# Performance work log

Measured on AMD Instinct MI355X. Metric: run time of the kernel, lower is better.

## Reference

```python
import jax, jax.numpy as jnp
import numpy as np

K = 4  # number of neighbors, per kNN-VC convention

def setup_inputs() -> dict:
    key = jax.random.key(0)
    k1, k2 = jax.random.split(key)
    source_feats = jax.random.normal(k1, (2048, 1024), dtype=jnp.float32)
    target_feats = jax.random.normal(k2, (50000, 1024), dtype=jnp.float32)
    return {"source_feats": source_feats, "target_feats": target_feats}

def reference(source_feats, target_feats):
    # cosine kNN matching: for each source frame, find K nearest target frames
    # under cosine distance (= highest cosine similarity), then average them.
    eps = jnp.asarray(1e-8, source_feats.dtype)
    src_n = source_feats / jnp.maximum(jnp.linalg.norm(source_feats, axis=-1, keepdims=True), eps)
    tgt_n = target_feats / jnp.maximum(jnp.linalg.norm(target_feats, axis=-1, keepdims=True), eps)
    # [T_src, T_tgt] cosine similarity
    sims = jnp.einsum('sd,td->st', src_n, tgt_n)
    _, idx = jax.lax.top_k(sims, K)          # [T_src, K]
    neighbors = target_feats[idx]             # [T_src, K, D]
    out = jnp.mean(neighbors, axis=1)         # [T_src, D]
    return out
```

## Files before the change

kernel.cpp:

```cpp
#include <hip/hip_runtime.h>
#include <math.h>

#define S_ROWS 2048
#define T_ROWS 50000
#define DIM    1024
#define KNN    4

#define BM 128
#define BN 128
#define KBB 128
#define TILES_PER_CHUNK 4
#define CHUNK_COLS (BN * TILES_PER_CHUNK)
#define NUM_CHUNKS ((T_ROWS + CHUNK_COLS - 1) / CHUNK_COLS)
#define T_PAD (NUM_CHUNKS * CHUNK_COLS)
#define NCAND (NUM_CHUNKS * KNN)
#define REFINE 16
#define SP 67
#define QSCALE 500.0f

typedef unsigned int uint;
typedef unsigned long long u64;
typedef signed char i8;
typedef __attribute__((ext_vector_type(4))) int i32x4;

__device__ __forceinline__ u64 packI(int v, int idx) {
  return ((u64)((uint)v ^ 0x80000000u) << 32) | (uint)(~idx);
}

template <int N>
__device__ __forceinline__ void insU(u64 p, u64 (&tv)[N]) {
  if (p <= tv[N - 1]) return;
  tv[N - 1] = p;
#pragma unroll
  for (int j = N - 1; j > 0; --j) {
    if (tv[j] > tv[j - 1]) { u64 t = tv[j]; tv[j] = tv[j - 1]; tv[j - 1] = t; }
  }
}

__device__ __forceinline__ void llds16(const void* g, void* l) {
  __builtin_amdgcn_global_load_lds(
      reinterpret_cast<__attribute__((address_space(1))) void*>(
          reinterpret_cast<uintptr_t>(g)),
      reinterpret_cast<__attribute__((address_space(3))) void*>(
          (unsigned)reinterpret_cast<uintptr_t>(l)),
      16, 0, 0);
}

__device__ __forceinline__ int imax2(int a, int b) { return a > b ? a : b; }

__global__ __launch_bounds__(256) void quant_kernel(const float* __restrict__ in,
                                                    i8* __restrict__ outq, int nvalid) {
  const int row = blockIdx.x;
  const int tid = threadIdx.x;
  if (row >= nvalid) {
    ((uint*)(outq + ((size_t)row << 10)))[tid] = 0u;
    return;
  }
  __shared__ float red[4];
  float4 v = ((const float4*)(in + ((size_t)row << 10)))[tid];
  float s = v.x * v.x + v.y * v.y + v.z * v.z + v.w * v.w;
#pragma unroll
  for (int off = 32; off; off >>= 1) s += __shfl_down(s, off, 64);
  if ((tid & 63) == 0) red[tid >> 6] = s;
  __syncthreads();
  float tot = red[0] + red[1] + red[2] + red[3];
  float r = QSCALE / fmaxf(sqrtf(tot), 1e-8f);
  int q0 = __float2int_rn(v.x * r), q1 = __float2int_rn(v.y * r);
  int q2 = __float2int_rn(v.z * r), q3 = __float2int_rn(v.w * r);
  q0 = imax2(-127, (q0 < 127 ? q0 : 127));
  q1 = imax2(-127, (q1 < 127 ? q1 : 127));
  q2 = imax2(-127, (q2 < 127 ? q2 : 127));
  q3 = imax2(-127, (q3 < 127 ? q3 : 127));
  uint packed = ((uint)q0 & 255u) | (((uint)q1 & 255u) << 8) |
                (((uint)q2 & 255u) << 16) | (((uint)q3 & 255u) << 24);
  ((uint*)(outq + ((size_t)row << 10)))[tid] = packed;
}

union __align__(16) SimSmem {
  i8 ab[2][BM * KBB];
  int sims[BM * SP];
  u64 mb[256 * KNN];
};

__global__ __launch_bounds__(256) void sim_i8_kernel(const i8* __restrict__ srcq,
                                                     const i8* __restrict__ tgtq,
                                                     u64* __restrict__ partials) {
  __shared__ SimSmem sm;
  i8* sA = sm.ab[0];
  i8* sB = sm.ab[1];

  const int tid = threadIdx.x;
  const int lane = tid & 63;
  const int wave = tid >> 6;
  const int qr = (wave >> 1) * 64;
  const int qch = wave & 1;
  const int m = lane & 15;
  const int quad = lane >> 4;
  const int r0 = blockIdx.x * BM;
  const int chunk = blockIdx.y;

  const int srow8 = lane >> 3;
  const int scb = (lane & 7) ^ srow8;
  const i8* aBase = srcq + (((size_t)(r0 + wave * 32 + srow8)) << 10) + scb * 16;
  i8* aL = sA + wave * 4096;
  i8* bL = sB + wave * 4096;

  const int axor = m & 7;
  const int aoff = (qr + m) * KBB;
  const int boff = (qch * 64 + m) * KBB;

  u64 topp[KNN] = {0, 0, 0, 0};
  int thrI = (int)0x80000000;

  for (int tile = 0; tile < TILES_PER_CHUNK; ++tile) {
    const int c0 = chunk * CHUNK_COLS + tile * BN;
    const i8* bBase = tgtq + (((size_t)(c0 + wave * 32 + srow8)) << 10) + scb * 16;

    i32x4 acc[4][4];
#pragma unroll
    for (int i = 0; i < 4; ++i)
#pragma unroll
      for (int j = 0; j < 4; ++j) acc[i][j] = (i32x4){0, 0, 0, 0};

    for (int kb = 0; kb < DIM; kb += KBB) {
#pragma unroll
      for (int d = 0; d < 4; ++d) {
        llds16(aBase + kb + d * 8192, aL + d * 1024);
        llds16(bBase + kb + d * 8192, bL + d * 1024);
      }
      __syncthreads();
#pragma unroll
      for (int s = 0; s < 2; ++s) {
        const int bpos = ((s * 4 + quad) ^ axor) * 16;
        i32x4 af[4], bf[4];
#pragma unroll
        for (int i = 0; i < 4; ++i)
          af[i] = *(const i32x4*)(sA + aoff + i * (16 * KBB) + bpos);
#pragma unroll
        for (int j = 0; j < 4; ++j)
          bf[j] = *(const i32x4*)(sB + boff + j * (16 * KBB) + bpos);
#pragma unroll
        for (int i = 0; i < 4; ++i)
#pragma unroll
          for (int j = 0; j < 4; ++j)
            acc[i][j] = __builtin_amdgcn_mfma_i32_16x16x64_i8(af[i], bf[j], acc[i][j], 0, 0, 0);
      }
      __syncthreads();
    }

#pragma unroll
    for (int ph = 0; ph < 2; ++ph) {
      if (qch == ph) {
#pragma unroll
        for (int i = 0; i < 4; ++i)
#pragma unroll
          for (int j = 0; j < 4; ++j)
#pragma unroll
            for (int reg = 0; reg < 4; ++reg)
              sm.sims[(qr + i * 16 + quad * 4 + reg) * SP + j * 16 + m] = acc[i][j][reg];
      }
      __syncthreads();
      {
        const int rowl = tid & 127;
        const int chh = tid >> 7;
        const int* srow = &sm.sims[rowl * SP + chh * 32];
        const int gbase = c0 + ph * 64 + chh * 32;
#pragma unroll
        for (int c = 0; c < 32; c += 4) {
          int a = srow[c], b = srow[c + 1], d2 = srow[c + 2], e = srow[c + 3];
          int mx = imax2(imax2(a, b), imax2(d2, e));
          if (mx > thrI) {
            const int g = gbase + c;
            if (g + 0 < T_ROWS) insU<KNN>(packI(a, g + 0), topp);
            if (g + 1 < T_ROWS) insU<KNN>(packI(b, g + 1), topp);
            if (g + 2 < T_ROWS) insU<KNN>(packI(d2, g + 2), topp);
            if (g + 3 < T_ROWS) insU<KNN>(packI(e, g + 3), topp);
            thrI = (int)((uint)(topp[KNN - 1] >> 32) ^ 0x80000000u);
          }
        }
      }
      __syncthreads();
    }
  }

#pragma unroll
  for (int j = 0; j < KNN; ++j) sm.mb[tid * KNN + j] = topp[j];
  __syncthreads();
  if (tid < 128) {
#pragma unroll
    for (int j = 0; j < KNN; ++j) insU<KNN>(sm.mb[(tid + 128) * KNN + j], topp);
    u64* dst = partials + ((size_t)(r0 + tid) * NUM_CHUNKS + chunk) * KNN;
#pragma unroll
    for (int j = 0; j < KNN; ++j) dst[j] = topp[j];
  }
}

__global__ __launch_bounds__(256) void merge_gather_kernel(
    const u64* __restrict__ partials, const float* __restrict__ src,
    const float* __restrict__ tgt, float* __restrict__ out) {
  const int row = blockIdx.x;
  const int tid = threadIdx.x;
  const int lane = tid & 63;
  const int wave = tid >> 6;
  __shared__ u64 cbuf[NCAND];
  __shared__ u64 part8[8][REFINE];
  __shared__ int cand[REFINE];
  __shared__ double cval[REFINE];
  __shared__ int fin[KNN];

  for (int c = tid; c < NCAND; c += 256) cbuf[c] = partials[(size_t)row * NCAND + c];
  __syncthreads();

  if (tid < 8) {
    u64 t16[REFINE];
#pragma unroll
    for (int j = 0; j < REFINE; ++j) t16[j] = 0;
    const int base = tid * (NCAND / 8);
    for (int c = 0; c < NCAND / 8; ++c) insU<REFINE>(cbuf[base + c], t16);
#pragma unroll
    for (int j = 0; j < REFINE; ++j) part8[tid][j] = t16[j];
  }
  __syncthreads();
  if (tid == 0) {
    u64 t16[REFINE];
#pragma unroll
    for (int j = 0; j < REFINE; ++j) t16[j] = 0;
    for (int s = 0; s < 8; ++s)
#pragma unroll
      for (int j = 0; j < REFINE; ++j) insU<REFINE>(part8[s][j], t16);
#pragma unroll
    for (int j = 0; j < REFINE; ++j) cand[j] = (int)(~(uint)t16[j]);
  }
  __syncthreads();

  const float4* s4 = (const float4*)(src + ((size_t)row << 10));
  float4 s0 = s4[lane], s1 = s4[lane + 64], s2 = s4[lane + 128], s3 = s4[lane + 192];
  double ss = (double)s0.x * s0.x + (double)s0.y * s0.y + (double)s0.z * s0.z + (double)s0.w * s0.w
            + (double)s1.x * s1.x + (double)s1.y * s1.y + (double)s1.z * s1.z + (double)s1.w * s1.w
            + (double)s2.x * s2.x + (double)s2.y * s2.y + (double)s2.z * s2.z + (double)s2.w * s2.w
            + (double)s3.x * s3.x + (double)s3.y * s3.y + (double)s3.z * s3.z + (double)s3.w * s3.w;
#pragma unroll
  for (int off = 32; off; off >>= 1) ss += __shfl_down(ss, off, 64);
  ss = __shfl(ss, 0, 64);
  const double sn = fmax(sqrt(ss), 1e-8);

  for (int cc = wave; cc < REFINE; cc += 4) {
    const float4* t4 = (const float4*)(tgt + ((size_t)cand[cc] << 10));
    float4 t0 = t4[lane], t1 = t4[lane + 64], t2 = t4[lane + 128], t3 = t4[lane + 192];
    double dd = (double)s0.x * t0.x + (double)s0.y * t0.y + (double)s0.z * t0.z + (double)s0.w * t0.w
              + (double)s1.x * t1.x + (double)s1.y * t1.y + (double)s1.z * t1.z + (double)s1.w * t1.w
              + (double)s2.x * t2.x + (double)s2.y * t2.y + (double)s2.z * t2.z + (double)s2.w * t2.w
              + (double)s3.x * t3.x + (double)s3.y * t3.y + (double)s3.z * t3.z + (double)s3.w * t3.w;
    double tt = (double)t0.x * t0.x + (double)t0.y * t0.y + (double)t0.z * t0.z + (double)t0.w * t0.w
              + (double)t1.x * t1.x + (double)t1.y * t1.y + (double)t1.z * t1.z + (double)t1.w * t1.w
              + (double)t2.x * t2.x + (double)t2.y * t2.y + (double)t2.z * t2.z + (double)t2.w * t2.w
              + (double)t3.x * t3.x + (double)t3.y * t3.y + (double)t3.z * t3.z + (double)t3.w * t3.w;
#pragma unroll
    for (int off = 32; off; off >>= 1) {
      dd += __shfl_down(dd, off, 64);
      tt += __shfl_down(tt, off, 64);
    }
    if (lane == 0) cval[cc] = dd / (sn * fmax(sqrt(tt), 1e-8));
  }
  __syncthreads();

  if (tid == 0) {
    bool used[REFINE];
#pragma unroll
    for (int j = 0; j < REFINE; ++j) used[j] = false;
    for (int k = 0; k < KNN; ++k) {
      int bj = -1; double bv = 0.0; int bidx = 0x7fffffff;
      for (int j = 0; j < REFINE; ++j) {
        if (used[j]) continue;
        if (bj < 0 || cval[j] > bv || (cval[j] == bv && cand[j] < bidx)) {
          bj = j; bv = cval[j]; bidx = cand[j];
        }
      }
      used[bj] = true;
      fin[k] = cand[bj];
    }
  }
  __syncthreads();

  const int d = tid * 4;
  float4 a = *(const float4*)(tgt + ((size_t)fin[0] << 10) + d);
  float4 b = *(const float4*)(tgt + ((size_t)fin[1] << 10) + d);
  float4 c = *(const float4*)(tgt + ((size_t)fin[2] << 10) + d);
  float4 e = *(const float4*)(tgt + ((size_t)fin[3] << 10) + d);
  float4 o;
  o.x = 0.25f * (a.x + b.x + c.x + e.x);
  o.y = 0.25f * (a.y + b.y + c.y + e.y);
  o.z = 0.25f * (a.z + b.z + c.z + e.z);
  o.w = 0.25f * (a.w + b.w + c.w + e.w);
  *(float4*)(out + ((size_t)row << 10) + d) = o;
}

extern "C" void kernel_launch(void* const* d_in, const int* in_sizes, int n_in,
                              void* d_out, int out_size, void* d_ws, size_t ws_size,
                              hipStream_t stream) {
  const float* src = (const float*)d_in[0];
  const float* tgt = (const float*)d_in[1];
  float* out = (float*)d_out;
  char* ws = (char*)d_ws;

  const size_t SRCQ_B = (size_t)S_ROWS << 10;
  const size_t TGTQ_B = (size_t)T_PAD << 10;

  i8* srcq = (i8*)ws;
  i8* tgtq = (i8*)(ws + SRCQ_B);
  u64* partials = (u64*)(ws + SRCQ_B + TGTQ_B);

  quant_kernel<<<S_ROWS, 256, 0, stream>>>(src, srcq, S_ROWS);
  quant_kernel<<<T_PAD, 256, 0, stream>>>(tgt, tgtq, T_ROWS);

  dim3 g3(S_ROWS / BM, NUM_CHUNKS);
  sim_i8_kernel<<<g3, 256, 0, stream>>>(srcq, tgtq, partials);

  merge_gather_kernel<<<S_ROWS, 256, 0, stream>>>(partials, src, tgt, out);
}
```

Measured before the change: 646.4 us.

## Double-buffer int8 GEMM K-loop with 64-wide slabs and MFMA priority boost

Replaces the single-buffered 128-wide K staging with two 64-wide shared-memory slabs. The load of the next slab is issued before computing on the current one, so global-to-LDS loads overlap with MFMA work. The swizzle is changed to match the 64-byte row stride, and s_setprio is raised around the MFMA blocks. Each slab now does half the MFMA work per barrier, and the correctness of the overlap depends on the llds load semantics and barrier placement.

```diff
diff --git a/kernel.cpp b/kernel.cpp
--- a/kernel.cpp
+++ b/kernel.cpp
@@ -8,7 +8,8 @@
 
 #define BM 128
 #define BN 128
-#define KBB 128
+#define KSL 64
+#define NSLAB (DIM / KSL)
 #define TILES_PER_CHUNK 4
 #define CHUNK_COLS (BN * TILES_PER_CHUNK)
 #define NUM_CHUNKS ((T_ROWS + CHUNK_COLS - 1) / CHUNK_COLS)
@@ -77,17 +78,38 @@
 }
 
 union __align__(16) SimSmem {
-  i8 ab[2][BM * KBB];
+  i8 ab[2][2 * BM * KSL];
   int sims[BM * SP];
   u64 mb[256 * KNN];
 };
+
+__device__ __forceinline__ void stage64(const i8* aP, const i8* bP, i8* aL, i8* bL) {
+  llds16(aP, aL);
+  llds16(aP + 16384, aL + 1024);
+  llds16(bP, bL);
+  llds16(bP + 16384, bL + 1024);
+}
+
+__device__ __forceinline__ void compute64(const i8* base, int aoff0, int boff0,
+                                          i32x4 (&acc)[4][4]) {
+  i32x4 af[4], bf[4];
+#pragma unroll
+  for (int i = 0; i < 4; ++i) af[i] = *(const i32x4*)(base + aoff0 + i * 1024);
+#pragma unroll
+  for (int j = 0; j < 4; ++j) bf[j] = *(const i32x4*)(base + 8192 + boff0 + j * 1024);
+  __builtin_amdgcn_s_setprio(1);
+#pragma unroll
+  for (int i = 0; i < 4; ++i)
+#pragma unroll
+    for (int j = 0; j < 4; ++j)
+      acc[i][j] = __builtin_amdgcn_mfma_i32_16x16x64_i8(af[i], bf[j], acc[i][j], 0, 0, 0);
+  __builtin_amdgcn_s_setprio(0);
+}
 
 __global__ __launch_bounds__(256) void sim_i8_kernel(const i8* __restrict__ srcq,
                                                      const i8* __restrict__ tgtq,
                                                      u64* __restrict__ partials) {
   __shared__ SimSmem sm;
-  i8* sA = sm.ab[0];
-  i8* sB = sm.ab[1];
 
   const int tid = threadIdx.x;
   const int lane = tid & 63;
@@ -99,22 +121,24 @@
   const int r0 = blockIdx.x * BM;
   const int chunk = blockIdx.y;
 
-  const int srow8 = lane >> 3;
-  const int scb = (lane & 7) ^ srow8;
-  const i8* aBase = srcq + (((size_t)(r0 + wave * 32 + srow8)) << 10) + scb * 16;
-  i8* aL = sA + wave * 4096;
-  i8* bL = sB + wave * 4096;
-
-  const int axor = m & 7;
-  const int aoff = (qr + m) * KBB;
-  const int boff = (qch * 64 + m) * KBB;
+  const int srow4 = lane >> 2;
+  const int scb4 = (lane & 3) ^ (srow4 & 3);
+  const i8* aLane = srcq + (((size_t)(r0 + wave * 32 + srow4)) << 10) + scb4 * 16;
+
+  const int swz = (quad ^ (m & 3)) << 4;
+  const int aoff0 = ((qr + m) << 6) + swz;
+  const int boff0 = ((qch * 64 + m) << 6) + swz;
 
   u64 topp[KNN] = {0, 0, 0, 0};
   int thrI = (int)0x80000000;
 
   for (int tile = 0; tile < TILES_PER_CHUNK; ++tile) {
     const int c0 = chunk * CHUNK_COLS + tile * BN;
-    const i8* bBase = tgtq + (((size_t)(c0 + wave * 32 + srow8)) << 10) + scb * 16;
+    const i8* bLane = tgtq + (((size_t)(c0 + wave * 32 + srow4)) << 10) + scb4 * 16;
+    i8* aL0 = sm.ab[0] + wave * 2048;
+    i8* bL0 = sm.ab[0] + 8192 + wave * 2048;
+    i8* aL1 = sm.ab[1] + wave * 2048;
+    i8* bL1 = sm.ab[1] + 8192 + wave * 2048;
 
     i32x4 acc[4][4];
 #pragma unroll
@@ -122,29 +146,16 @@
 #pragma unroll
       for (int j = 0; j < 4; ++j) acc[i][j] = (i32x4){0, 0, 0, 0};
 
-    for (int kb = 0; kb < DIM; kb += KBB) {
-#pragma unroll
-      for (int d = 0; d < 4; ++d) {
-        llds16(aBase + kb + d * 8192, aL + d * 1024);
-        llds16(bBase + kb + d * 8192, bL + d * 1024);
-      }
+    stage64(aLane, bLane, aL0, bL0);
+    __syncthreads();
+
+    for (int u = 0; u < NSLAB; u += 2) {
+      stage64(aLane + ((u + 1) << 6), bLane + ((u + 1) << 6), aL1, bL1);
+      compute64(sm.ab[0], aoff0, boff0, acc);
       __syncthreads();
-#pragma unroll
-      for (int s = 0; s < 2; ++s) {
-        const int bpos = ((s * 4 + quad) ^ axor) * 16;
-        i32x4 af[4], bf[4];
-#pragma unroll
-        for (int i = 0; i < 4; ++i)
-          af[i] = *(const i32x4*)(sA + aoff + i * (16 * KBB) + bpos);
-#pragma unroll
-        for (int j = 0; j < 4; ++j)
-          bf[j] = *(const i32x4*)(sB + boff + j * (16 * KBB) + bpos);
-#pragma unroll
-        for (int i = 0; i < 4; ++i)
-#pragma unroll
-          for (int j = 0; j < 4; ++j)
-            acc[i][j] = __builtin_amdgcn_mfma_i32_16x16x64_i8(af[i], bf[j], acc[i][j], 0, 0, 0);
-      }
+      if (u + 2 < NSLAB)
+        stage64(aLane + ((u + 2) << 6), bLane + ((u + 2) << 6), aL0, bL0);
+      compute64(sm.ab[1], aoff0, boff0, acc);
       __syncthreads();
     }
 
```

New measurement: 647.5 us. Within noise of the previous version (+0.2%).
